# Performance work log

Hardware: AMD Instinct MI355X
Metric: run time of the kernel (lower is better)

The kernel has to match this reference:

```python
import jax, jax.numpy as jnp
import numpy as np

N_NODES = 40000
FEAT = 128
HID = 128
EMB = 64
N_EDGES = 640000


def setup_inputs() -> dict:
    key = jax.random.key(0)
    ks = jax.random.split(key, 8)
    x = jax.random.normal(ks[0], (N_NODES, FEAT), dtype=jnp.float32)
    edge_index = jax.random.randint(ks[1], (2, N_EDGES), 0, N_NODES, dtype=jnp.int64)
    s1 = 1.0 / np.sqrt(FEAT)
    s2 = 1.0 / np.sqrt(HID)
    W1_l = jax.random.uniform(ks[2], (HID, FEAT), jnp.float32, -s1, s1)
    b1 = jax.random.uniform(ks[3], (HID,), jnp.float32, -s1, s1)
    W1_r = jax.random.uniform(ks[4], (HID, FEAT), jnp.float32, -s1, s1)
    W2_l = jax.random.uniform(ks[5], (EMB, HID), jnp.float32, -s2, s2)
    b2 = jax.random.uniform(ks[6], (EMB,), jnp.float32, -s2, s2)
    W2_r = jax.random.uniform(ks[7], (EMB, HID), jnp.float32, -s2, s2)
    return {"x": x, "edge_index": edge_index, "W1_l": W1_l, "b1": b1,
            "W1_r": W1_r, "W2_l": W2_l, "b2": b2, "W2_r": W2_r}


def _sage_conv(x, src, dst, W_l, b_l, W_r, n_nodes):
    # mean aggregation of source-node features onto destination nodes
    msg = x[src]                                           # [E, d]
    agg = jax.ops.segment_sum(msg, dst, num_segments=n_nodes)   # [N, d]
    cnt = jax.ops.segment_sum(jnp.ones((src.shape[0],), x.dtype), dst,
                              num_segments=n_nodes)        # [N]
    agg = agg / jnp.maximum(cnt, 1.0)[:, None]
    # out = lin_l(mean_j x_j) + lin_r(x_i); bias lives in lin_l
    return agg @ W_l.T + b_l + x @ W_r.T


def reference(x, edge_index, W1_l, b1, W1_r, W2_l, b2, W2_r):
    src, dst = edge_index[0], edge_index[1]
    n = x.shape[0]
    h = _sage_conv(x, src, dst, W1_l, b1, W1_r, n)
    h = jax.nn.elu(h)
    # dropout p=0.2 is identity in eval mode
    h = _sage_conv(h, src, dst, W2_l, b2, W2_r, n)
    return jax.nn.log_softmax(h, axis=1)
```

## Files before the change

kernel.cpp:

```cpp
#include <hip/hip_runtime.h>
#include <hip/hip_fp16.h>
#include <math.h>

#define N_NODES 40000
#define FEATD 128
#define EMB 64
#define N_EDGES 640000
#define CAP 64

typedef unsigned short u16;
typedef __attribute__((ext_vector_type(8))) unsigned short u16x8;
typedef __attribute__((ext_vector_type(8))) _Float16 f16x8;
typedef __attribute__((ext_vector_type(4))) float f32x4;

__device__ __forceinline__ float h2f(u16 h) {
  __half hh;
  *(u16*)&hh = h;
  return __half2float(hh);
}
__device__ __forceinline__ u16 f2h(float f) {
  __half hh = __float2half(f);
  return *(u16*)&hh;
}

__global__ __launch_bounds__(256) void prep_kernel(
    const float* __restrict__ x, const float* __restrict__ W1l,
    const float* __restrict__ W1r, const float* __restrict__ W2l,
    const float* __restrict__ W2r, u16* __restrict__ xh,
    u16* __restrict__ wp) {
  int bid = blockIdx.x;
  if (bid < 2500) {
    int i = bid * 256 + threadIdx.x;
    float4 v0 = *(const float4*)(&x[i * 8]);
    float4 v1 = *(const float4*)(&x[i * 8 + 4]);
    u16x8 o;
    o[0] = f2h(v0.x); o[1] = f2h(v0.y); o[2] = f2h(v0.z); o[3] = f2h(v0.w);
    o[4] = f2h(v1.x); o[5] = f2h(v1.y); o[6] = f2h(v1.z); o[7] = f2h(v1.w);
    *(u16x8*)(&xh[i * 8]) = o;
  } else {
    int i = (bid - 2500) * 256 + threadIdx.x;
    const float* srcp;
    int off;
    if (i < 16384)      { srcp = W1l; off = i; }
    else if (i < 32768) { srcp = W1r; off = i - 16384; }
    else if (i < 40960) { srcp = W2l; off = i - 32768; }
    else                { srcp = W2r; off = i - 40960; }
    wp[i] = f2h(srcp[off]);
  }
}

__global__ __launch_bounds__(256) void fill_kernel(
    const int* __restrict__ src, const int* __restrict__ dst,
    int* __restrict__ deg, u16* __restrict__ bucket) {
  int t = blockIdx.x * 256 + threadIdx.x;
  int4 s4 = *(const int4*)(&src[t * 4]);
  int4 d4 = *(const int4*)(&dst[t * 4]);
  int p0 = atomicAdd(&deg[d4.x], 1);
  int p1 = atomicAdd(&deg[d4.y], 1);
  int p2 = atomicAdd(&deg[d4.z], 1);
  int p3 = atomicAdd(&deg[d4.w], 1);
  if (p0 < CAP) bucket[d4.x * CAP + p0] = (u16)s4.x;
  if (p1 < CAP) bucket[d4.y * CAP + p1] = (u16)s4.y;
  if (p2 < CAP) bucket[d4.z * CAP + p2] = (u16)s4.z;
  if (p3 < CAP) bucket[d4.w * CAP + p3] = (u16)s4.w;
}

__global__ __launch_bounds__(256) void gather_mean_f16(
    const u16* __restrict__ xh, const int* __restrict__ deg,
    const u16* __restrict__ bucket, u16* __restrict__ aggh) {
  int n = blockIdx.x * 4 + (threadIdx.x >> 6);
  int lane = threadIdx.x & 63;
  int g = lane >> 4;
  int li = lane & 15;
  int dgf = deg[n];
  int dg = dgf < CAP ? dgf : CAP;
  float inv = 1.0f / fmaxf((float)dgf, 1.0f);
  const u16* bk = bucket + n * CAP;
  float acc0[8], acc1[8];
#pragma unroll
  for (int i = 0; i < 8; i++) { acc0[i] = 0.f; acc1[i] = 0.f; }
  int d = g;
  for (; d + 4 < dg; d += 8) {
    u16x8 v0 = *(const u16x8*)(&xh[(int)bk[d] * 128 + li * 8]);
    u16x8 v1 = *(const u16x8*)(&xh[(int)bk[d + 4] * 128 + li * 8]);
#pragma unroll
    for (int i = 0; i < 8; i++) { acc0[i] += h2f(v0[i]); acc1[i] += h2f(v1[i]); }
  }
  if (d < dg) {
    u16x8 v0 = *(const u16x8*)(&xh[(int)bk[d] * 128 + li * 8]);
#pragma unroll
    for (int i = 0; i < 8; i++) acc0[i] += h2f(v0[i]);
  }
#pragma unroll
  for (int i = 0; i < 8; i++) {
    acc0[i] += acc1[i];
    acc0[i] += __shfl_xor(acc0[i], 16);
    acc0[i] += __shfl_xor(acc0[i], 32);
  }
  if (g == 0) {
    u16x8 o;
#pragma unroll
    for (int i = 0; i < 8; i++) o[i] = f2h(acc0[i] * inv);
    *(u16x8*)(&aggh[n * 128 + li * 8]) = o;
  }
}

__global__ __launch_bounds__(256) void gemm12_kernel(
    const u16* __restrict__ AggH, const u16* __restrict__ XH,
    const u16* __restrict__ wp, const float* __restrict__ b1v,
    const float* __restrict__ b2v, u16* __restrict__ Yh,
    float* __restrict__ Z) {
  const u16* w1l = wp;
  const u16* w1r = wp + 16384;
  const u16* w2l = wp + 32768;
  const u16* w2r = wp + 40960;

  __shared__ __align__(16) union {
    struct {
      u16 wl[128][72], wr[128][72];
      u16 a[64][72], x[64][72];
    } p1;
    struct {
      u16 h[64][136];
      u16 w2l[64][136], w2r[64][136];
    } p2;
  } L;

  const int tid = threadIdx.x;
  const int wv = tid >> 6;
  const int lane = tid & 63;
  const int li = lane & 15;
  const int q = lane >> 4;
  const int nbase = blockIdx.x * 64;

  f32x4 acc1[8];
#pragma unroll
  for (int jt = 0; jt < 8; jt++) acc1[jt] = (f32x4){0.f, 0.f, 0.f, 0.f};

  for (int kb = 0; kb < 2; kb++) {
#pragma unroll
    for (int it = 0; it < 4; it++) {
      int idx = tid + 256 * it;
      int j = idx >> 3, c = idx & 7;
      int go = j * 128 + kb * 64 + c * 8;
      *(u16x8*)(&L.p1.wl[j][c * 8]) = *(const u16x8*)(&w1l[go]);
      *(u16x8*)(&L.p1.wr[j][c * 8]) = *(const u16x8*)(&w1r[go]);
    }
#pragma unroll
    for (int it = 0; it < 2; it++) {
      int idx = tid + 256 * it;
      int n = idx >> 3, c = idx & 7;
      int go = (nbase + n) * 128 + kb * 64 + c * 8;
      *(u16x8*)(&L.p1.a[n][c * 8]) = *(const u16x8*)(&AggH[go]);
      *(u16x8*)(&L.p1.x[n][c * 8]) = *(const u16x8*)(&XH[go]);
    }
    __syncthreads();
#pragma unroll
    for (int kk = 0; kk < 2; kk++) {
      f16x8 aF = *(const f16x8*)(&L.p1.a[wv * 16 + li][kk * 32 + q * 8]);
      f16x8 xF = *(const f16x8*)(&L.p1.x[wv * 16 + li][kk * 32 + q * 8]);
#pragma unroll
      for (int jt = 0; jt < 8; jt++) {
        f16x8 wlF = *(const f16x8*)(&L.p1.wl[jt * 16 + li][kk * 32 + q * 8]);
        f16x8 wrF = *(const f16x8*)(&L.p1.wr[jt * 16 + li][kk * 32 + q * 8]);
        acc1[jt] = __builtin_amdgcn_mfma_f32_16x16x32_f16(aF, wlF, acc1[jt], 0, 0, 0);
        acc1[jt] = __builtin_amdgcn_mfma_f32_16x16x32_f16(xF, wrF, acc1[jt], 0, 0, 0);
      }
    }
    __syncthreads();
  }

#pragma unroll
  for (int jt = 0; jt < 8; jt++) {
    int j = jt * 16 + li;
    float bb = b1v[j];
#pragma unroll
    for (int r = 0; r < 4; r++) {
      float v = acc1[jt][r] + bb;
      v = v > 0.f ? v : expm1f(v);
      L.p2.h[wv * 16 + q * 4 + r][j] = f2h(v);
    }
  }
#pragma unroll
  for (int it = 0; it < 4; it++) {
    int idx = tid + 256 * it;
    int j = idx >> 4, c = idx & 15;
    int go = j * 128 + c * 8;
    *(u16x8*)(&L.p2.w2l[j][c * 8]) = *(const u16x8*)(&w2l[go]);
    *(u16x8*)(&L.p2.w2r[j][c * 8]) = *(const u16x8*)(&w2r[go]);
  }
  __syncthreads();

  f32x4 accY[4], accZ[4];
#pragma unroll
  for (int mt = 0; mt < 4; mt++) {
    accY[mt] = (f32x4){0.f, 0.f, 0.f, 0.f};
    accZ[mt] = (f32x4){0.f, 0.f, 0.f, 0.f};
  }
#pragma unroll
  for (int kc = 0; kc < 4; kc++) {
    f16x8 blF = *(const f16x8*)(&L.p2.w2l[wv * 16 + li][kc * 32 + q * 8]);
    f16x8 brF = *(const f16x8*)(&L.p2.w2r[wv * 16 + li][kc * 32 + q * 8]);
#pragma unroll
    for (int mt = 0; mt < 4; mt++) {
      f16x8 hF = *(const f16x8*)(&L.p2.h[mt * 16 + li][kc * 32 + q * 8]);
      accY[mt] = __builtin_amdgcn_mfma_f32_16x16x32_f16(hF, blF, accY[mt], 0, 0, 0);
      accZ[mt] = __builtin_amdgcn_mfma_f32_16x16x32_f16(hF, brF, accZ[mt], 0, 0, 0);
    }
  }

  {
    int j2 = wv * 16 + li;
    float bb = b2v[j2];
#pragma unroll
    for (int mt = 0; mt < 4; mt++) {
#pragma unroll
      for (int r = 0; r < 4; r++) {
        int node = nbase + mt * 16 + q * 4 + r;
        Yh[node * 64 + j2] = f2h(accY[mt][r]);
        Z[node * 64 + j2] = accZ[mt][r] + bb;
      }
    }
  }
}

__global__ __launch_bounds__(256) void final_kernel(
    const u16* __restrict__ Y, const float* __restrict__ Z,
    const int* __restrict__ deg, const u16* __restrict__ bucket,
    float* __restrict__ out) {
  int n = blockIdx.x * 4 + (threadIdx.x >> 6);
  int lane = threadIdx.x & 63;
  int g = lane >> 4;
  int li = lane & 15;
  int dgf = deg[n];
  int dg = dgf < CAP ? dgf : CAP;
  float inv = 1.0f / fmaxf((float)dgf, 1.0f);
  const u16* bk = bucket + n * CAP;
  float4 acc = {0.f, 0.f, 0.f, 0.f};
  float4 accB = {0.f, 0.f, 0.f, 0.f};
  int d = g;
  for (; d + 4 < dg; d += 8) {
    ushort4 v0 = *(const ushort4*)(&Y[(int)bk[d] * 64 + li * 4]);
    ushort4 v1 = *(const ushort4*)(&Y[(int)bk[d + 4] * 64 + li * 4]);
    acc.x += h2f(v0.x); acc.y += h2f(v0.y); acc.z += h2f(v0.z); acc.w += h2f(v0.w);
    accB.x += h2f(v1.x); accB.y += h2f(v1.y); accB.z += h2f(v1.z); accB.w += h2f(v1.w);
  }
  if (d < dg) {
    ushort4 v0 = *(const ushort4*)(&Y[(int)bk[d] * 64 + li * 4]);
    acc.x += h2f(v0.x); acc.y += h2f(v0.y); acc.z += h2f(v0.z); acc.w += h2f(v0.w);
  }
  acc.x += accB.x; acc.y += accB.y; acc.z += accB.z; acc.w += accB.w;
  acc.x += __shfl_xor(acc.x, 16); acc.y += __shfl_xor(acc.y, 16);
  acc.z += __shfl_xor(acc.z, 16); acc.w += __shfl_xor(acc.w, 16);
  acc.x += __shfl_xor(acc.x, 32); acc.y += __shfl_xor(acc.y, 32);
  acc.z += __shfl_xor(acc.z, 32); acc.w += __shfl_xor(acc.w, 32);
  float4 zb = *(const float4*)(&Z[n * 64 + li * 4]);
  float4 v;
  v.x = zb.x + acc.x * inv; v.y = zb.y + acc.y * inv;
  v.z = zb.z + acc.z * inv; v.w = zb.w + acc.w * inv;
  float m = fmaxf(fmaxf(v.x, v.y), fmaxf(v.z, v.w));
  m = fmaxf(m, __shfl_xor(m, 1)); m = fmaxf(m, __shfl_xor(m, 2));
  m = fmaxf(m, __shfl_xor(m, 4)); m = fmaxf(m, __shfl_xor(m, 8));
  float s = __expf(v.x - m) + __expf(v.y - m) + __expf(v.z - m) + __expf(v.w - m);
  s += __shfl_xor(s, 1); s += __shfl_xor(s, 2);
  s += __shfl_xor(s, 4); s += __shfl_xor(s, 8);
  float lg = m + logf(s);
  if (lane < 16) {
    float4 o = {v.x - lg, v.y - lg, v.z - lg, v.w - lg};
    *(float4*)(&out[n * 64 + li * 4]) = o;
  }
}

extern "C" void kernel_launch(void* const* d_in, const int* in_sizes, int n_in,
                              void* d_out, int out_size, void* d_ws, size_t ws_size,
                              hipStream_t stream) {
  const float* x   = (const float*)d_in[0];
  const int*   ei  = (const int*)d_in[1];
  const float* W1l = (const float*)d_in[2];
  const float* b1  = (const float*)d_in[3];
  const float* W1r = (const float*)d_in[4];
  const float* W2l = (const float*)d_in[5];
  const float* b2  = (const float*)d_in[6];
  const float* W2r = (const float*)d_in[7];
  float* out = (float*)d_out;

  const int* src = ei;
  const int* dst = ei + N_EDGES;

  u16* bucket = (u16*)d_ws;
  int* deg = (int*)(bucket + (size_t)N_NODES * CAP);
  u16* xh = (u16*)(deg + N_NODES);
  u16* aggh = xh + (size_t)N_NODES * FEATD;
  u16* yh = aggh + (size_t)N_NODES * FEATD;
  float* z = (float*)(yh + (size_t)N_NODES * EMB);
  u16* wp = (u16*)(z + (size_t)N_NODES * EMB);

  hipMemsetAsync(deg, 0, N_NODES * sizeof(int), stream);
  prep_kernel<<<2500 + 192, 256, 0, stream>>>(x, W1l, W1r, W2l, W2r, xh, wp);
  fill_kernel<<<N_EDGES / 4 / 256, 256, 0, stream>>>(src, dst, deg, bucket);

  gather_mean_f16<<<N_NODES / 4, 256, 0, stream>>>(xh, deg, bucket, aggh);
  gemm12_kernel<<<N_NODES / 64, 256, 0, stream>>>(aggh, xh, wp, b1, b2, yh, z);
  final_kernel<<<N_NODES / 4, 256, 0, stream>>>(yh, z, deg, bucket, out);
}
```

Measured before the change: 183.9 us.

## Fuse prep and fill kernels, unroll gather further, widen final-kernel loads

Merges the fp16 conversion kernel and the edge bucket-fill kernel into one launch, with fill blocks placed first so atomics overlap the conversion work. The layer-1 gather now uses four independent accumulators to keep more loads in flight. The final kernel switches to 8 lanes per row with 16-byte loads and 8 edge groups per wavefront, which shortens the softmax reductions. The main costs are higher register use in the gather and one extra shuffle stage in the final reduction.

```diff
diff --git a/kernel.cpp b/kernel.cpp
--- a/kernel.cpp
+++ b/kernel.cpp
@@ -23,14 +23,27 @@
   return *(u16*)&hh;
 }
 
-__global__ __launch_bounds__(256) void prep_kernel(
+__global__ __launch_bounds__(256) void prep_fill_kernel(
     const float* __restrict__ x, const float* __restrict__ W1l,
     const float* __restrict__ W1r, const float* __restrict__ W2l,
-    const float* __restrict__ W2r, u16* __restrict__ xh,
-    u16* __restrict__ wp) {
+    const float* __restrict__ W2r, const int* __restrict__ src,
+    const int* __restrict__ dst, u16* __restrict__ xh,
+    u16* __restrict__ wp, int* __restrict__ deg, u16* __restrict__ bucket) {
   int bid = blockIdx.x;
-  if (bid < 2500) {
-    int i = bid * 256 + threadIdx.x;
+  if (bid < 625) {
+    int t = bid * 256 + threadIdx.x;
+    int4 s4 = *(const int4*)(&src[t * 4]);
+    int4 d4 = *(const int4*)(&dst[t * 4]);
+    int p0 = atomicAdd(&deg[d4.x], 1);
+    int p1 = atomicAdd(&deg[d4.y], 1);
+    int p2 = atomicAdd(&deg[d4.z], 1);
+    int p3 = atomicAdd(&deg[d4.w], 1);
+    if (p0 < CAP) bucket[d4.x * CAP + p0] = (u16)s4.x;
+    if (p1 < CAP) bucket[d4.y * CAP + p1] = (u16)s4.y;
+    if (p2 < CAP) bucket[d4.z * CAP + p2] = (u16)s4.z;
+    if (p3 < CAP) bucket[d4.w * CAP + p3] = (u16)s4.w;
+  } else if (bid < 3125) {
+    int i = (bid - 625) * 256 + threadIdx.x;
     float4 v0 = *(const float4*)(&x[i * 8]);
     float4 v1 = *(const float4*)(&x[i * 8 + 4]);
     u16x8 o;
@@ -38,7 +51,7 @@
     o[4] = f2h(v1.x); o[5] = f2h(v1.y); o[6] = f2h(v1.z); o[7] = f2h(v1.w);
     *(u16x8*)(&xh[i * 8]) = o;
   } else {
-    int i = (bid - 2500) * 256 + threadIdx.x;
+    int i = (bid - 3125) * 256 + threadIdx.x;
     const float* srcp;
     int off;
     if (i < 16384)      { srcp = W1l; off = i; }
@@ -47,22 +60,6 @@
     else                { srcp = W2r; off = i - 40960; }
     wp[i] = f2h(srcp[off]);
   }
-}
-
-__global__ __launch_bounds__(256) void fill_kernel(
-    const int* __restrict__ src, const int* __restrict__ dst,
-    int* __restrict__ deg, u16* __restrict__ bucket) {
-  int t = blockIdx.x * 256 + threadIdx.x;
-  int4 s4 = *(const int4*)(&src[t * 4]);
-  int4 d4 = *(const int4*)(&dst[t * 4]);
-  int p0 = atomicAdd(&deg[d4.x], 1);
-  int p1 = atomicAdd(&deg[d4.y], 1);
-  int p2 = atomicAdd(&deg[d4.z], 1);
-  int p3 = atomicAdd(&deg[d4.w], 1);
-  if (p0 < CAP) bucket[d4.x * CAP + p0] = (u16)s4.x;
-  if (p1 < CAP) bucket[d4.y * CAP + p1] = (u16)s4.y;
-  if (p2 < CAP) bucket[d4.z * CAP + p2] = (u16)s4.z;
-  if (p3 < CAP) bucket[d4.w * CAP + p3] = (u16)s4.w;
 }
 
 __global__ __launch_bounds__(256) void gather_mean_f16(
@@ -76,10 +73,21 @@
   int dg = dgf < CAP ? dgf : CAP;
   float inv = 1.0f / fmaxf((float)dgf, 1.0f);
   const u16* bk = bucket + n * CAP;
-  float acc0[8], acc1[8];
-#pragma unroll
-  for (int i = 0; i < 8; i++) { acc0[i] = 0.f; acc1[i] = 0.f; }
+  float acc0[8], acc1[8], acc2[8], acc3[8];
+#pragma unroll
+  for (int i = 0; i < 8; i++) { acc0[i] = 0.f; acc1[i] = 0.f; acc2[i] = 0.f; acc3[i] = 0.f; }
   int d = g;
+  for (; d + 12 < dg; d += 16) {
+    u16x8 v0 = *(const u16x8*)(&xh[(int)bk[d] * 128 + li * 8]);
+    u16x8 v1 = *(const u16x8*)(&xh[(int)bk[d + 4] * 128 + li * 8]);
+    u16x8 v2 = *(const u16x8*)(&xh[(int)bk[d + 8] * 128 + li * 8]);
+    u16x8 v3 = *(const u16x8*)(&xh[(int)bk[d + 12] * 128 + li * 8]);
+#pragma unroll
+    for (int i = 0; i < 8; i++) {
+      acc0[i] += h2f(v0[i]); acc1[i] += h2f(v1[i]);
+      acc2[i] += h2f(v2[i]); acc3[i] += h2f(v3[i]);
+    }
+  }
   for (; d + 4 < dg; d += 8) {
     u16x8 v0 = *(const u16x8*)(&xh[(int)bk[d] * 128 + li * 8]);
     u16x8 v1 = *(const u16x8*)(&xh[(int)bk[d + 4] * 128 + li * 8]);
@@ -93,7 +101,7 @@
   }
 #pragma unroll
   for (int i = 0; i < 8; i++) {
-    acc0[i] += acc1[i];
+    acc0[i] += acc1[i] + acc2[i] + acc3[i];
     acc0[i] += __shfl_xor(acc0[i], 16);
     acc0[i] += __shfl_xor(acc0[i], 32);
   }
@@ -230,44 +238,57 @@
     float* __restrict__ out) {
   int n = blockIdx.x * 4 + (threadIdx.x >> 6);
   int lane = threadIdx.x & 63;
-  int g = lane >> 4;
-  int li = lane & 15;
+  int g = lane >> 3;
+  int li = lane & 7;
   int dgf = deg[n];
   int dg = dgf < CAP ? dgf : CAP;
   float inv = 1.0f / fmaxf((float)dgf, 1.0f);
   const u16* bk = bucket + n * CAP;
-  float4 acc = {0.f, 0.f, 0.f, 0.f};
-  float4 accB = {0.f, 0.f, 0.f, 0.f};
+  float acc0[8], acc1[8];
+#pragma unroll
+  for (int i = 0; i < 8; i++) { acc0[i] = 0.f; acc1[i] = 0.f; }
   int d = g;
-  for (; d + 4 < dg; d += 8) {
-    ushort4 v0 = *(const ushort4*)(&Y[(int)bk[d] * 64 + li * 4]);
-    ushort4 v1 = *(const ushort4*)(&Y[(int)bk[d + 4] * 64 + li * 4]);
-    acc.x += h2f(v0.x); acc.y += h2f(v0.y); acc.z += h2f(v0.z); acc.w += h2f(v0.w);
-    accB.x += h2f(v1.x); accB.y += h2f(v1.y); accB.z += h2f(v1.z); accB.w += h2f(v1.w);
+  for (; d + 8 < dg; d += 16) {
+    u16x8 v0 = *(const u16x8*)(&Y[(int)bk[d] * 64 + li * 8]);
+    u16x8 v1 = *(const u16x8*)(&Y[(int)bk[d + 8] * 64 + li * 8]);
+#pragma unroll
+    for (int i = 0; i < 8; i++) { acc0[i] += h2f(v0[i]); acc1[i] += h2f(v1[i]); }
   }
   if (d < dg) {
-    ushort4 v0 = *(const ushort4*)(&Y[(int)bk[d] * 64 + li * 4]);
-    acc.x += h2f(v0.x); acc.y += h2f(v0.y); acc.z += h2f(v0.z); acc.w += h2f(v0.w);
-  }
-  acc.x += accB.x; acc.y += accB.y; acc.z += accB.z; acc.w += accB.w;
-  acc.x += __shfl_xor(acc.x, 16); acc.y += __shfl_xor(acc.y, 16);
-  acc.z += __shfl_xor(acc.z, 16); acc.w += __shfl_xor(acc.w, 16);
-  acc.x += __shfl_xor(acc.x, 32); acc.y += __shfl_xor(acc.y, 32);
-  acc.z += __shfl_xor(acc.z, 32); acc.w += __shfl_xor(acc.w, 32);
-  float4 zb = *(const float4*)(&Z[n * 64 + li * 4]);
-  float4 v;
-  v.x = zb.x + acc.x * inv; v.y = zb.y + acc.y * inv;
-  v.z = zb.z + acc.z * inv; v.w = zb.w + acc.w * inv;
-  float m = fmaxf(fmaxf(v.x, v.y), fmaxf(v.z, v.w));
-  m = fmaxf(m, __shfl_xor(m, 1)); m = fmaxf(m, __shfl_xor(m, 2));
-  m = fmaxf(m, __shfl_xor(m, 4)); m = fmaxf(m, __shfl_xor(m, 8));
-  float s = __expf(v.x - m) + __expf(v.y - m) + __expf(v.z - m) + __expf(v.w - m);
-  s += __shfl_xor(s, 1); s += __shfl_xor(s, 2);
-  s += __shfl_xor(s, 4); s += __shfl_xor(s, 8);
+    u16x8 v0 = *(const u16x8*)(&Y[(int)bk[d] * 64 + li * 8]);
+#pragma unroll
+    for (int i = 0; i < 8; i++) acc0[i] += h2f(v0[i]);
+  }
+#pragma unroll
+  for (int i = 0; i < 8; i++) {
+    acc0[i] += acc1[i];
+    acc0[i] += __shfl_xor(acc0[i], 8);
+    acc0[i] += __shfl_xor(acc0[i], 16);
+    acc0[i] += __shfl_xor(acc0[i], 32);
+  }
+  float4 zb0 = *(const float4*)(&Z[n * 64 + li * 8]);
+  float4 zb1 = *(const float4*)(&Z[n * 64 + li * 8 + 4]);
+  float v[8];
+  v[0] = zb0.x + acc0[0] * inv; v[1] = zb0.y + acc0[1] * inv;
+  v[2] = zb0.z + acc0[2] * inv; v[3] = zb0.w + acc0[3] * inv;
+  v[4] = zb1.x + acc0[4] * inv; v[5] = zb1.y + acc0[5] * inv;
+  v[6] = zb1.z + acc0[6] * inv; v[7] = zb1.w + acc0[7] * inv;
+  float m = v[0];
+#pragma unroll
+  for (int i = 1; i < 8; i++) m = fmaxf(m, v[i]);
+  m = fmaxf(m, __shfl_xor(m, 1));
+  m = fmaxf(m, __shfl_xor(m, 2));
+  m = fmaxf(m, __shfl_xor(m, 4));
+  float s = 0.f;
+#pragma unroll
+  for (int i = 0; i < 8; i++) s += __expf(v[i] - m);
+  s += __shfl_xor(s, 1); s += __shfl_xor(s, 2); s += __shfl_xor(s, 4);
   float lg = m + logf(s);
-  if (lane < 16) {
-    float4 o = {v.x - lg, v.y - lg, v.z - lg, v.w - lg};
-    *(float4*)(&out[n * 64 + li * 4]) = o;
+  if (lane < 8) {
+    float4 o0 = {v[0] - lg, v[1] - lg, v[2] - lg, v[3] - lg};
+    float4 o1 = {v[4] - lg, v[5] - lg, v[6] - lg, v[7] - lg};
+    *(float4*)(&out[n * 64 + li * 8]) = o0;
+    *(float4*)(&out[n * 64 + li * 8 + 4]) = o1;
   }
 }
 
@@ -296,9 +317,8 @@
   u16* wp = (u16*)(z + (size_t)N_NODES * EMB);
 
   hipMemsetAsync(deg, 0, N_NODES * sizeof(int), stream);
-  prep_kernel<<<2500 + 192, 256, 0, stream>>>(x, W1l, W1r, W2l, W2r, xh, wp);
-  fill_kernel<<<N_EDGES / 4 / 256, 256, 0, stream>>>(src, dst, deg, bucket);
-
+  prep_fill_kernel<<<3317, 256, 0, stream>>>(x, W1l, W1r, W2l, W2r, src, dst,
+                                             xh, wp, deg, bucket);
   gather_mean_f16<<<N_NODES / 4, 256, 0, stream>>>(xh, deg, bucket, aggh);
   gemm12_kernel<<<N_NODES / 64, 256, 0, stream>>>(aggh, xh, wp, b1, b2, yh, z);
   final_kernel<<<N_NODES / 4, 256, 0, stream>>>(yh, z, deg, bucket, out);
```

Result: no change. 181.3 us (-1.4%).
